# Kernel tuning notes

Hardware: AMD Instinct MI355X
Metric: run time of the kernel (lower is better)

Reference implementation:

```python
import jax, jax.numpy as jnp
import numpy as np

B, S, D, H = 8, 1024, 1024, 16
DH = D // H  # 64
SCALE = (DH // H) ** (-0.5)  # faithful to torch: (key.size(-1) // num_heads) ** -0.5 = 4**-0.5 = 0.5
LN_EPS = 1e-5


def setup_inputs() -> dict:
    key = jax.random.key(0)
    ks = jax.random.split(key, 12)
    f = jnp.float32
    return {
        "key":   jax.random.normal(ks[0], (B, S, D), f),
        "value": jax.random.normal(ks[1], (B, S, D), f),
        "query": jax.random.normal(ks[2], (B, S, D), f),
        "Wq": jax.random.normal(ks[3], (D, D), f) * 0.02,
        "bq": jnp.zeros((D,), f),
        "Wk": jax.random.normal(ks[4], (D, D), f) * 0.02,
        "bk": jnp.zeros((D,), f),
        "Wv": jax.random.normal(ks[5], (D, D), f) * 0.02,
        "bv": jnp.zeros((D,), f),
        "Wo": jax.random.normal(ks[6], (D, D), f) * 0.02,
        "bo": jnp.zeros((D,), f),
        "ln_gamma": jnp.ones((D,), f),
        "ln_beta": jnp.zeros((D,), f),
    }


def _layer_norm(x, gamma, beta):
    mu = jnp.mean(x, axis=-1, keepdims=True)
    var = jnp.mean(jnp.square(x - mu), axis=-1, keepdims=True)
    return (x - mu) * jax.lax.rsqrt(var + LN_EPS) * gamma + beta


def reference(key, value, query, Wq, bq, Wk, bk, Wv, bv, Wo, bo, ln_gamma, ln_beta):
    residual = query
    # QKV projections (torch Linear: x @ W.T + b)
    k = key @ Wk.T + bk
    v = value @ Wv.T + bv
    q = query @ Wq.T + bq
    # Faithful raw view [B,S,H*dh] -> [B*H, S, dh] (row-major reshape, as in torch .view)
    k = k.reshape(B * H, S, DH)
    v = v.reshape(B * H, S, DH)
    q = q.reshape(B * H, S, DH)
    # scores: [B*H, S, S], softmax over last axis (dim=2)
    attn = jnp.einsum("bid,bjd->bij", q, k) * SCALE
    attn = jax.nn.softmax(attn, axis=2)
    context = jnp.einsum("bij,bjd->bid", attn, v)
    context = context.reshape(B, S, D)  # faithful raw view back
    out = context @ Wo.T + bo
    out = _layer_norm(residual + out, ln_gamma, ln_beta)
    return out, attn
```

## Files before the change

kernel.cpp:

```cpp
#include <hip/hip_runtime.h>
#include <stdint.h>

typedef unsigned short ushort_t;
typedef __attribute__((ext_vector_type(8))) short s16x8;
typedef __attribute__((ext_vector_type(8))) unsigned short u16x8;
typedef __attribute__((ext_vector_type(4))) unsigned short u16x4;
typedef __attribute__((ext_vector_type(4))) float f32x4;

#define AS1C(p) ((const __attribute__((address_space(1))) void*)(p))
#define AS3(p)  ((__attribute__((address_space(3))) void*)(p))

#define QSCALE 0.7213475204444817f

#define EXP2F(x) __builtin_amdgcn_exp2f(x)
#define LOG2F(x) __builtin_amdgcn_logf(x)

#define WAVE_LDS_FENCE()                                    \
  do {                                                      \
    asm volatile("s_waitcnt lgkmcnt(0)" ::: "memory");      \
    __builtin_amdgcn_sched_barrier(0);                      \
  } while (0)

#define SBAR()                                              \
  do {                                                      \
    __builtin_amdgcn_sched_barrier(0);                      \
    __builtin_amdgcn_s_barrier();                           \
    __builtin_amdgcn_sched_barrier(0);                      \
  } while (0)

__device__ __forceinline__ ushort_t f2bf(float f) {
  uint32_t u = __float_as_uint(f);
  u += 0x7fffu + ((u >> 16) & 1u);
  return (ushort_t)(u >> 16);
}
__device__ __forceinline__ float bf2f(ushort_t h) {
  return __uint_as_float(((uint32_t)h) << 16);
}

__global__ __launch_bounds__(256) void cvt3_kernel(const float* __restrict__ s0,
                                                   const float* __restrict__ s1,
                                                   const float* __restrict__ s2,
                                                   ushort_t* __restrict__ dst) {
  const int y = blockIdx.y;
  const float* src = y == 0 ? s0 : (y == 1 ? s1 : s2);
  const int i = blockIdx.x * 256 + threadIdx.x;
  const float4 v = ((const float4*)src)[i];
  ushort4 o;
  o.x = f2bf(v.x); o.y = f2bf(v.y); o.z = f2bf(v.z); o.w = f2bf(v.w);
  ((ushort4*)(dst + (size_t)y * 8388608))[i] = o;
}

__global__ __launch_bounds__(256) void cvtw_kernel(const float* __restrict__ w0,
                                                   const float* __restrict__ w1,
                                                   const float* __restrict__ w2,
                                                   const float* __restrict__ w3,
                                                   ushort_t* __restrict__ dqkv,
                                                   ushort_t* __restrict__ dwo) {
  const int y = blockIdx.y;
  const float* src = y == 0 ? w0 : (y == 1 ? w1 : (y == 2 ? w2 : w3));
  ushort_t* dst = y < 3 ? dqkv + (size_t)y * 1048576 : dwo;
  const float sc = y == 0 ? QSCALE : 1.0f;
  const int i = blockIdx.x * 256 + threadIdx.x;
  const float4 v = ((const float4*)src)[i];
  ushort4 o;
  o.x = f2bf(v.x * sc); o.y = f2bf(v.y * sc); o.z = f2bf(v.z * sc); o.w = f2bf(v.w * sc);
  ((ushort4*)dst)[i] = o;
}

__global__ __launch_bounds__(256) void biascat_kernel(const float* __restrict__ bq,
                                                      const float* __restrict__ bk,
                                                      const float* __restrict__ bv,
                                                      float* __restrict__ dst) {
  const int i = blockIdx.x * 256 + threadIdx.x;
  dst[i] = i < 1024 ? bq[i] * QSCALE : (i < 2048 ? bk[i - 1024] : bv[i - 2048]);
}

template <int OUT_BF16>
__global__ __launch_bounds__(512) void gemm_nt(const ushort_t* __restrict__ A0,
                                               const ushort_t* __restrict__ A1,
                                               const ushort_t* __restrict__ A2,
                                               const ushort_t* __restrict__ B,
                                               const float* __restrict__ bias,
                                               void* __restrict__ C0,
                                               void* __restrict__ C1,
                                               void* __restrict__ C2) {
  __shared__ ushort_t As[3][128 * 32];
  __shared__ ushort_t Bs[3][128 * 32];
  const int tid = threadIdx.x;
  const int w = tid >> 6, lane = tid & 63, g = lane >> 4, c = lane & 15;
  const int wm = w >> 1, wn = w & 1;
  const int m0 = blockIdx.y * 128, n0 = blockIdx.x * 128;
  const int sel = n0 >> 10, nloc0 = n0 & 1023;
  const ushort_t* A = sel == 0 ? A0 : (sel == 1 ? A1 : A2);
  char* C = (char*)(sel == 0 ? C0 : (sel == 1 ? C1 : C2));
  f32x4 acc[2][4] = {};

  const int srow = tid >> 2, scol = (tid & 3) << 3;
  const int sdst = (w * 64) * 8;

#define G_STAGE(buf, k0_)                                                                  \
  do {                                                                                     \
    __builtin_amdgcn_global_load_lds(AS1C(&A[(size_t)(m0 + srow) * 1024 + (k0_) + scol]),  \
                                     AS3(&As[buf][sdst]), 16, 0, 0);                       \
    __builtin_amdgcn_global_load_lds(AS1C(&B[(size_t)(n0 + srow) * 1024 + (k0_) + scol]),  \
                                     AS3(&Bs[buf][sdst]), 16, 0, 0);                       \
  } while (0)

  G_STAGE(0, 0);
  G_STAGE(1, 32);
  asm volatile("s_waitcnt vmcnt(2)" ::: "memory");
  SBAR();
  int cur = 0;
  for (int it = 0; it < 32; ++it) {
    if (it < 30) {
      const int sb = cur >= 1 ? cur - 1 : 2;
      G_STAGE(sb, 32 * (it + 2));
    }
    s16x8 af[2], bfr[4];
#pragma unroll
    for (int mi = 0; mi < 2; ++mi)
      af[mi] = *(const s16x8*)&As[cur][(wm * 32 + mi * 16 + c) * 32 + g * 8];
#pragma unroll
    for (int ni = 0; ni < 4; ++ni)
      bfr[ni] = *(const s16x8*)&Bs[cur][(wn * 64 + ni * 16 + c) * 32 + g * 8];
    __builtin_amdgcn_s_setprio(1);
#pragma unroll
    for (int mi = 0; mi < 2; ++mi)
#pragma unroll
      for (int ni = 0; ni < 4; ++ni)
        acc[mi][ni] = __builtin_amdgcn_mfma_f32_16x16x32_bf16(af[mi], bfr[ni], acc[mi][ni], 0, 0, 0);
    __builtin_amdgcn_s_setprio(0);
    if (it < 31) {
      if (it < 30)
        asm volatile("s_waitcnt vmcnt(2) lgkmcnt(0)" ::: "memory");
      else
        asm volatile("s_waitcnt vmcnt(0) lgkmcnt(0)" ::: "memory");
      SBAR();
    }
    cur = cur < 2 ? cur + 1 : 0;
  }
#undef G_STAGE

#pragma unroll
  for (int ni = 0; ni < 4; ++ni) {
    const int nn = wn * 64 + ni * 16 + c;
    const float bv = bias[n0 + nn];
#pragma unroll
    for (int mi = 0; mi < 2; ++mi) {
#pragma unroll
      for (int rr = 0; rr < 4; ++rr) {
        const int m = m0 + wm * 32 + mi * 16 + g * 4 + rr;
        const float val = acc[mi][ni][rr] + bv;
        if (OUT_BF16)
          ((ushort_t*)C)[(size_t)m * 1024 + nloc0 + nn] = f2bf(val);
        else
          ((float*)C)[(size_t)m * 1024 + nloc0 + nn] = val;
      }
    }
  }
}

__global__ __launch_bounds__(256) void transpose_v(const ushort_t* __restrict__ v,
                                                   ushort_t* __restrict__ vt) {
  __shared__ ushort_t T[64][72];
  const int n = blockIdx.y, ib = blockIdx.x;
  const int t = threadIdx.x;
  {
    const int row = t >> 2, cb = (t & 3) << 4;
    const ushort_t* src = v + (size_t)n * 65536 + (size_t)(ib * 64 + row) * 64 + cb;
    *(u16x8*)&T[row][cb] = *(const u16x8*)src;
    *(u16x8*)&T[row][cb + 8] = *(const u16x8*)(src + 8);
  }
  __syncthreads();
  {
    const int dh = t >> 2, ibs = (t & 3) << 4;
    u16x8 a, b;
#pragma unroll
    for (int e = 0; e < 8; ++e) { a[e] = T[ibs + e][dh]; b[e] = T[ibs + 8 + e][dh]; }
    ushort_t* dst = vt + (size_t)n * 65536 + (size_t)dh * 1024 + ib * 64 + ibs;
    *(u16x8*)dst = a;
    *(u16x8*)(dst + 8) = b;
  }
}

__global__ __launch_bounds__(256) void stats_kernel(const ushort_t* __restrict__ q,
                                                    const ushort_t* __restrict__ k,
                                                    float* __restrict__ bias_out) {
  __shared__ ushort_t Kb[3][64 * 64];
  const int wg = blockIdx.x;
  const int idx = ((wg & 7) << 7) | (wg >> 3);
  const int n = idx >> 3, qb = idx & 7;
  const int tid = threadIdx.x, w = tid >> 6, lane = tid & 63, g = lane >> 4, c = lane & 15;
  const int q0 = qb * 128 + w * 32;
  const ushort_t* qh = q + (size_t)n * 65536;
  const char* khb = (const char*)(k + (size_t)n * 65536);

  const int r0 = w * 16 + (lane >> 3);
  const int csw = (((lane & 7) ^ (lane >> 3)) << 4);

#define STAGE_KS(buf, jt_)                                                                  \
  do {                                                                                      \
    __builtin_amdgcn_global_load_lds(AS1C(khb + ((size_t)(jt_)*64 + r0) * 128 + csw),       \
                                     AS3(&Kb[buf][(w * 2 + 0) * 512]), 16, 0, 0);           \
    __builtin_amdgcn_global_load_lds(AS1C(khb + ((size_t)(jt_)*64 + r0 + 8) * 128 + csw),   \
                                     AS3(&Kb[buf][(w * 2 + 1) * 512]), 16, 0, 0);           \
  } while (0)
#define KFRAGS(buf, jn, h)                                                    \
  (*(const s16x8*)((const char*)&Kb[buf][0] +                                 \
                   (((((jn)*16 + c) * 128 + (h)*64 + g * 16)) ^ ((c & 7) << 4))))

  s16x8 aq[2][2];
#pragma unroll
  for (int fr = 0; fr < 2; ++fr) {
    aq[fr][0] = *(const s16x8*)&qh[(q0 + fr * 16 + c) * 64 + g * 8];
    aq[fr][1] = *(const s16x8*)&qh[(q0 + fr * 16 + c) * 64 + 32 + g * 8];
  }

  float l_acc[2][4] = {};

  STAGE_KS(0, 0);
  STAGE_KS(1, 1);
  asm volatile("s_waitcnt vmcnt(2)" ::: "memory");
  SBAR();
  int cur = 0;
  for (int jt = 0; jt < 16; ++jt) {
    if (jt < 14) {
      const int sb = cur >= 1 ? cur - 1 : 2;
      STAGE_KS(sb, jt + 2);
    }
    f32x4 sfr[2][4];
    __builtin_amdgcn_s_setprio(1);
#pragma unroll
    for (int fr = 0; fr < 2; ++fr)
#pragma unroll
      for (int jn = 0; jn < 4; ++jn) {
        f32x4 z = {0.f, 0.f, 0.f, 0.f};
        z = __builtin_amdgcn_mfma_f32_16x16x32_bf16(aq[fr][0], KFRAGS(cur, jn, 0), z, 0, 0, 0);
        z = __builtin_amdgcn_mfma_f32_16x16x32_bf16(aq[fr][1], KFRAGS(cur, jn, 1), z, 0, 0, 0);
        sfr[fr][jn] = z;
      }
    __builtin_amdgcn_s_setprio(0);
#pragma unroll
    for (int fr = 0; fr < 2; ++fr)
#pragma unroll
      for (int rr = 0; rr < 4; ++rr)
        l_acc[fr][rr] += EXP2F(sfr[fr][0][rr]) + EXP2F(sfr[fr][1][rr]) +
                         EXP2F(sfr[fr][2][rr]) + EXP2F(sfr[fr][3][rr]);
    if (jt < 15) {
      if (jt < 14)
        asm volatile("s_waitcnt vmcnt(2) lgkmcnt(0)" ::: "memory");
      else
        asm volatile("s_waitcnt vmcnt(0) lgkmcnt(0)" ::: "memory");
      SBAR();
    }
    cur = cur < 2 ? cur + 1 : 0;
  }

#pragma unroll
  for (int fr = 0; fr < 2; ++fr)
#pragma unroll
    for (int rr = 0; rr < 4; ++rr) {
      float l = l_acc[fr][rr];
      l += __shfl_xor(l, 1);
      l += __shfl_xor(l, 2);
      l += __shfl_xor(l, 4);
      l += __shfl_xor(l, 8);
      if (c == 0)
        bias_out[(size_t)n * 1024 + q0 + fr * 16 + g * 4 + rr] = LOG2F(l);
    }
#undef STAGE_KS
#undef KFRAGS
}

__global__ __launch_bounds__(256) void attn_kernel(const ushort_t* __restrict__ q,
                                                   const ushort_t* __restrict__ k,
                                                   const ushort_t* __restrict__ vt,
                                                   const float* __restrict__ stats,
                                                   float* __restrict__ attn,
                                                   ushort_t* __restrict__ ctx) {
  __shared__ ushort_t Kb[2][64 * 64];
  __shared__ ushort_t Vb[2][64 * 64];
  __shared__ ushort_t Pb[4][32 * 64];
  const int wg = blockIdx.x;
  const int idx = ((wg & 7) << 7) | (wg >> 3);
  const int n = idx >> 3, qb = idx & 7;
  const int tid = threadIdx.x, w = tid >> 6, lane = tid & 63, g = lane >> 4, c = lane & 15;
  const int i0 = qb * 128 + w * 32;
  const ushort_t* qh = q + (size_t)n * 65536;
  const char* khb = (const char*)(k + (size_t)n * 65536);
  const char* vhb = (const char*)(vt + (size_t)n * 65536);
  char* pwb = (char*)&Pb[w][0];

  const int r0 = w * 16 + (lane >> 3);
  const int csw = (((lane & 7) ^ (lane >> 3)) << 4);

#define STAGE_K(buf, jt_)                                                                   \
  do {                                                                                      \
    __builtin_amdgcn_global_load_lds(AS1C(khb + ((size_t)(jt_)*64 + r0) * 128 + csw),       \
                                     AS3(&Kb[buf][(w * 2 + 0) * 512]), 16, 0, 0);           \
    __builtin_amdgcn_global_load_lds(AS1C(khb + ((size_t)(jt_)*64 + r0 + 8) * 128 + csw),   \
                                     AS3(&Kb[buf][(w * 2 + 1) * 512]), 16, 0, 0);           \
  } while (0)
#define STAGE_V(buf, jt_)                                                                   \
  do {                                                                                      \
    __builtin_amdgcn_global_load_lds(AS1C(vhb + (size_t)r0 * 2048 + (jt_)*128 + csw),       \
                                     AS3(&Vb[buf][(w * 2 + 0) * 512]), 16, 0, 0);           \
    __builtin_amdgcn_global_load_lds(AS1C(vhb + (size_t)(r0 + 8) * 2048 + (jt_)*128 + csw), \
                                     AS3(&Vb[buf][(w * 2 + 1) * 512]), 16, 0, 0);           \
  } while (0)
#define KFRAG(buf, jn, h)                                                     \
  (*(const s16x8*)((const char*)&Kb[buf][0] +                                 \
                   (((((jn)*16 + c) * 128 + (h)*64 + g * 16)) ^ ((c & 7) << 4))))
#define VFRAG(buf, dn, ks_)                                                   \
  (*(const s16x8*)((const char*)&Vb[buf][0] +                                 \
                   (((((dn)*16 + c) * 128 + (ks_)*64 + g * 16)) ^ ((c & 7) << 4))))

  s16x8 aq[2][2];
  float bias_r[2][4];
#pragma unroll
  for (int fr = 0; fr < 2; ++fr) {
    aq[fr][0] = *(const s16x8*)&qh[(i0 + fr * 16 + c) * 64 + g * 8];
    aq[fr][1] = *(const s16x8*)&qh[(i0 + fr * 16 + c) * 64 + 32 + g * 8];
    const float* sb = stats + (size_t)n * 1024 + i0 + fr * 16;
#pragma unroll
    for (int r = 0; r < 4; ++r) bias_r[fr][r] = sb[4 * g + r];
  }

  f32x4 cacc[2][4] = {};
  float* arow = attn + (size_t)n * 1048576;

  STAGE_K(0, 0);
  STAGE_V(0, 0);
  asm volatile("s_waitcnt vmcnt(0) lgkmcnt(0)" ::: "memory");
  SBAR();
  for (int jt = 0; jt < 16; ++jt) {
    const int cur = jt & 1;
    if (jt < 15) { STAGE_K(cur ^ 1, jt + 1); STAGE_V(cur ^ 1, jt + 1); }
    f32x4 s[2][4];
    __builtin_amdgcn_s_setprio(1);
#pragma unroll
    for (int fr = 0; fr < 2; ++fr)
#pragma unroll
      for (int jn = 0; jn < 4; ++jn) {
        f32x4 z = {0.f, 0.f, 0.f, 0.f};
        z = __builtin_amdgcn_mfma_f32_16x16x32_bf16(aq[fr][0], KFRAG(cur, jn, 0), z, 0, 0, 0);
        z = __builtin_amdgcn_mfma_f32_16x16x32_bf16(aq[fr][1], KFRAG(cur, jn, 1), z, 0, 0, 0);
        s[fr][jn] = z;
      }
    __builtin_amdgcn_s_setprio(0);
#pragma unroll
    for (int fr = 0; fr < 2; ++fr)
#pragma unroll
      for (int jn = 0; jn < 4; ++jn)
#pragma unroll
        for (int r = 0; r < 4; ++r) {
          const float p = EXP2F(s[fr][jn][r] - bias_r[fr][r]);
          const int row = fr * 16 + 4 * g + r;
          const int A = (row << 7) + ((jn * 16 + c) << 1);
          *(ushort_t*)(pwb + (A ^ ((row & 7) << 4))) = f2bf(p);
        }
    WAVE_LDS_FENCE();
    __builtin_amdgcn_s_setprio(1);
#pragma unroll
    for (int ks = 0; ks < 2; ++ks) {
      s16x8 pa[2];
#pragma unroll
      for (int fr = 0; fr < 2; ++fr) {
        const int A = ((fr * 16 + c) << 7) + (ks << 6) + (g << 4);
        pa[fr] = *(const s16x8*)(pwb + (A ^ ((c & 7) << 4)));
      }
#pragma unroll
      for (int dn = 0; dn < 4; ++dn) {
        const s16x8 bv = VFRAG(cur, dn, ks);
        cacc[0][dn] = __builtin_amdgcn_mfma_f32_16x16x32_bf16(pa[0], bv, cacc[0][dn], 0, 0, 0);
        cacc[1][dn] = __builtin_amdgcn_mfma_f32_16x16x32_bf16(pa[1], bv, cacc[1][dn], 0, 0, 0);
      }
    }
    __builtin_amdgcn_s_setprio(0);
#pragma unroll
    for (int fr = 0; fr < 2; ++fr)
#pragma unroll
      for (int e = 0; e < 4; ++e) {
        const int row = fr * 16 + g + 4 * e;
        const int A = (row << 7) + (c << 3);
        const u16x4 hv = *(const u16x4*)(pwb + (A ^ ((row & 7) << 4)));
        f32x4 fv;
#pragma unroll
        for (int t2 = 0; t2 < 4; ++t2) fv[t2] = bf2f(hv[t2]);
        __builtin_nontemporal_store(
            fv, (f32x4*)&arow[(size_t)(i0 + row) * 1024 + jt * 64 + c * 4]);
      }
    if (jt < 15) {
      asm volatile("s_waitcnt vmcnt(8) lgkmcnt(0)" ::: "memory");
      SBAR();
    }
  }

  ushort_t* ch = ctx + (size_t)n * 65536;
#pragma unroll
  for (int fr = 0; fr < 2; ++fr)
#pragma unroll
    for (int dn = 0; dn < 4; ++dn)
#pragma unroll
      for (int r = 0; r < 4; ++r)
        ch[(size_t)(i0 + fr * 16 + 4 * g + r) * 64 + dn * 16 + c] = f2bf(cacc[fr][dn][r]);
#undef STAGE_K
#undef STAGE_V
#undef KFRAG
#undef VFRAG
}

__global__ __launch_bounds__(256) void ln_kernel(const float* __restrict__ proj,
                                                 const float* __restrict__ resid,
                                                 const float* __restrict__ gamma,
                                                 const float* __restrict__ beta,
                                                 float* __restrict__ out) {
  __shared__ float sred[4], ssred[4];
  const int row = blockIdx.x, t = threadIdx.x;
  const float4 pv = ((const float4*)(proj + (size_t)row * 1024))[t];
  const float4 rv = ((const float4*)(resid + (size_t)row * 1024))[t];
  float4 x;
  x.x = pv.x + rv.x; x.y = pv.y + rv.y; x.z = pv.z + rv.z; x.w = pv.w + rv.w;
  float s = x.x + x.y + x.z + x.w;
  float ss = x.x * x.x + x.y * x.y + x.z * x.z + x.w * x.w;
#pragma unroll
  for (int msk = 1; msk < 64; msk <<= 1) {
    s += __shfl_xor(s, msk);
    ss += __shfl_xor(ss, msk);
  }
  const int w = t >> 6, lane = t & 63;
  if (lane == 0) { sred[w] = s; ssred[w] = ss; }
  __syncthreads();
  s = sred[0] + sred[1] + sred[2] + sred[3];
  ss = ssred[0] + ssred[1] + ssred[2] + ssred[3];
  const float mu = s * (1.f / 1024.f);
  const float var = ss * (1.f / 1024.f) - mu * mu;
  const float rs = rsqrtf(var + 1e-5f);
  const float4 gm = ((const float4*)gamma)[t];
  const float4 bt = ((const float4*)beta)[t];
  float4 o;
  o.x = (x.x - mu) * rs * gm.x + bt.x;
  o.y = (x.y - mu) * rs * gm.y + bt.y;
  o.z = (x.z - mu) * rs * gm.z + bt.z;
  o.w = (x.w - mu) * rs * gm.w + bt.w;
  ((float4*)(out + (size_t)row * 1024))[t] = o;
}

extern "C" void kernel_launch(void* const* d_in, const int* in_sizes, int n_in,
                              void* d_out, int out_size, void* d_ws, size_t ws_size,
                              hipStream_t stream) {
  const float* key   = (const float*)d_in[0];
  const float* value = (const float*)d_in[1];
  const float* query = (const float*)d_in[2];
  const float* Wq = (const float*)d_in[3];  const float* bq = (const float*)d_in[4];
  const float* Wk = (const float*)d_in[5];  const float* bk = (const float*)d_in[6];
  const float* Wv = (const float*)d_in[7];  const float* bv = (const float*)d_in[8];
  const float* Wo = (const float*)d_in[9];  const float* bo = (const float*)d_in[10];
  const float* gamma = (const float*)d_in[11];
  const float* beta  = (const float*)d_in[12];

  char* ws = (char*)d_ws;
  ushort_t* q_   = (ushort_t*)(ws + 0);
  ushort_t* k_   = (ushort_t*)(ws + 16777216);
  ushort_t* vt_  = (ushort_t*)(ws + 33554432);
  ushort_t* ctx_ = (ushort_t*)(ws + 50331648);
  ushort_t* wo_  = (ushort_t*)(ws + 67108864);
  float*    proj_ = (float*)(ws + 0);

  char* o8 = (char*)d_out;
  float*    outp  = (float*)o8;
  float*    attnp = (float*)(o8 + 33554432);
  float*    stats = (float*)o8;
  ushort_t* xq   = (ushort_t*)(o8 + 33554432);
  ushort_t* xk   = (ushort_t*)(o8 + 50331648);
  ushort_t* xv   = (ushort_t*)(o8 + 67108864);
  ushort_t* wqkv = (ushort_t*)(o8 + 83886080);
  ushort_t* v_   = (ushort_t*)(o8 + 90177536);
  float*    bqkv = (float*)(o8 + 106954752);

  cvt3_kernel<<<dim3(8192, 3), 256, 0, stream>>>(query, key, value, xq);
  cvtw_kernel<<<dim3(1024, 4), 256, 0, stream>>>(Wq, Wk, Wv, Wo, wqkv, wo_);
  biascat_kernel<<<12, 256, 0, stream>>>(bq, bk, bv, bqkv);

  gemm_nt<1><<<dim3(24, 64), 512, 0, stream>>>(xq, xk, xv, wqkv, bqkv, q_, k_, v_);

  transpose_v<<<dim3(16, 128), 256, 0, stream>>>(v_, vt_);

  stats_kernel<<<1024, 256, 0, stream>>>(q_, k_, stats);

  attn_kernel<<<1024, 256, 0, stream>>>(q_, k_, vt_, stats, attnp, ctx_);

  gemm_nt<0><<<dim3(8, 64), 512, 0, stream>>>(ctx_, ctx_, ctx_, wo_, bo, proj_, proj_, proj_);

  ln_kernel<<<8192, 256, 0, stream>>>(proj_, query, gamma, beta, outp);
}
```

Baseline: 314.0 us.

## Swap MFMA operands so P stays in registers, double stats tile

In the attention kernel the QK^T MFMA operands are swapped, so each lane holds a row's scores along the key dimension. The probabilities are written straight to the attn output as fp32 vectors and packed to bf16, then rearranged with cross-lane shuffles into the B operand of the PV MFMA (also with swapped operands). This removes the per-wave LDS P buffer, the LDS round-trip and the bf16 readback for the attn store, and the attn output now keeps full fp32 precision instead of bf16-rounded values. Separately, the stats kernel handles 64 query rows per wave with half as many blocks, reusing each staged K tile across more rows.

Measured after the change: 392.3 us. 1.25x slower.

```diff
diff --git a/kernel.cpp b/kernel.cpp
--- a/kernel.cpp
+++ b/kernel.cpp
@@ -6,6 +6,7 @@
 typedef __attribute__((ext_vector_type(8))) unsigned short u16x8;
 typedef __attribute__((ext_vector_type(4))) unsigned short u16x4;
 typedef __attribute__((ext_vector_type(4))) float f32x4;
+typedef __attribute__((ext_vector_type(4))) unsigned int u32x4;
 
 #define AS1C(p) ((const __attribute__((address_space(1))) void*)(p))
 #define AS3(p)  ((__attribute__((address_space(3))) void*)(p))
@@ -14,12 +15,6 @@
 
 #define EXP2F(x) __builtin_amdgcn_exp2f(x)
 #define LOG2F(x) __builtin_amdgcn_logf(x)
-
-#define WAVE_LDS_FENCE()                                    \
-  do {                                                      \
-    asm volatile("s_waitcnt lgkmcnt(0)" ::: "memory");      \
-    __builtin_amdgcn_sched_barrier(0);                      \
-  } while (0)
 
 #define SBAR()                                              \
   do {                                                      \
@@ -33,8 +28,8 @@
   u += 0x7fffu + ((u >> 16) & 1u);
   return (ushort_t)(u >> 16);
 }
-__device__ __forceinline__ float bf2f(ushort_t h) {
-  return __uint_as_float(((uint32_t)h) << 16);
+__device__ __forceinline__ uint32_t packbf(float lo, float hi) {
+  return (uint32_t)f2bf(lo) | ((uint32_t)f2bf(hi) << 16);
 }
 
 __global__ __launch_bounds__(256) void cvt3_kernel(const float* __restrict__ s0,
@@ -188,10 +183,10 @@
                                                     float* __restrict__ bias_out) {
   __shared__ ushort_t Kb[3][64 * 64];
   const int wg = blockIdx.x;
-  const int idx = ((wg & 7) << 7) | (wg >> 3);
-  const int n = idx >> 3, qb = idx & 7;
+  const int idx = ((wg & 7) << 6) | (wg >> 3);
+  const int n = idx >> 2, qb = idx & 3;
   const int tid = threadIdx.x, w = tid >> 6, lane = tid & 63, g = lane >> 4, c = lane & 15;
-  const int q0 = qb * 128 + w * 32;
+  const int q0 = qb * 256 + w * 64;
   const ushort_t* qh = q + (size_t)n * 65536;
   const char* khb = (const char*)(k + (size_t)n * 65536);
 
@@ -209,14 +204,14 @@
   (*(const s16x8*)((const char*)&Kb[buf][0] +                                 \
                    (((((jn)*16 + c) * 128 + (h)*64 + g * 16)) ^ ((c & 7) << 4))))
 
-  s16x8 aq[2][2];
-#pragma unroll
-  for (int fr = 0; fr < 2; ++fr) {
+  s16x8 aq[4][2];
+#pragma unroll
+  for (int fr = 0; fr < 4; ++fr) {
     aq[fr][0] = *(const s16x8*)&qh[(q0 + fr * 16 + c) * 64 + g * 8];
     aq[fr][1] = *(const s16x8*)&qh[(q0 + fr * 16 + c) * 64 + 32 + g * 8];
   }
 
-  float l_acc[2][4] = {};
+  float l_acc[4][4] = {};
 
   STAGE_KS(0, 0);
   STAGE_KS(1, 1);
@@ -228,24 +223,23 @@
       const int sb = cur >= 1 ? cur - 1 : 2;
       STAGE_KS(sb, jt + 2);
     }
-    f32x4 sfr[2][4];
-    __builtin_amdgcn_s_setprio(1);
-#pragma unroll
-    for (int fr = 0; fr < 2; ++fr)
+#pragma unroll
+    for (int fr = 0; fr < 4; ++fr) {
+      f32x4 sfr[4];
+      __builtin_amdgcn_s_setprio(1);
 #pragma unroll
       for (int jn = 0; jn < 4; ++jn) {
         f32x4 z = {0.f, 0.f, 0.f, 0.f};
         z = __builtin_amdgcn_mfma_f32_16x16x32_bf16(aq[fr][0], KFRAGS(cur, jn, 0), z, 0, 0, 0);
         z = __builtin_amdgcn_mfma_f32_16x16x32_bf16(aq[fr][1], KFRAGS(cur, jn, 1), z, 0, 0, 0);
-        sfr[fr][jn] = z;
+        sfr[jn] = z;
       }
-    __builtin_amdgcn_s_setprio(0);
-#pragma unroll
-    for (int fr = 0; fr < 2; ++fr)
+      __builtin_amdgcn_s_setprio(0);
 #pragma unroll
       for (int rr = 0; rr < 4; ++rr)
-        l_acc[fr][rr] += EXP2F(sfr[fr][0][rr]) + EXP2F(sfr[fr][1][rr]) +
-                         EXP2F(sfr[fr][2][rr]) + EXP2F(sfr[fr][3][rr]);
+        l_acc[fr][rr] += EXP2F(sfr[0][rr]) + EXP2F(sfr[1][rr]) +
+                         EXP2F(sfr[2][rr]) + EXP2F(sfr[3][rr]);
+    }
     if (jt < 15) {
       if (jt < 14)
         asm volatile("s_waitcnt vmcnt(2) lgkmcnt(0)" ::: "memory");
@@ -257,7 +251,7 @@
   }
 
 #pragma unroll
-  for (int fr = 0; fr < 2; ++fr)
+  for (int fr = 0; fr < 4; ++fr)
 #pragma unroll
     for (int rr = 0; rr < 4; ++rr) {
       float l = l_acc[fr][rr];
@@ -280,7 +274,6 @@
                                                    ushort_t* __restrict__ ctx) {
   __shared__ ushort_t Kb[2][64 * 64];
   __shared__ ushort_t Vb[2][64 * 64];
-  __shared__ ushort_t Pb[4][32 * 64];
   const int wg = blockIdx.x;
   const int idx = ((wg & 7) << 7) | (wg >> 3);
   const int n = idx >> 3, qb = idx & 7;
@@ -289,7 +282,6 @@
   const ushort_t* qh = q + (size_t)n * 65536;
   const char* khb = (const char*)(k + (size_t)n * 65536);
   const char* vhb = (const char*)(vt + (size_t)n * 65536);
-  char* pwb = (char*)&Pb[w][0];
 
   const int r0 = w * 16 + (lane >> 3);
   const int csw = (((lane & 7) ^ (lane >> 3)) << 4);
@@ -316,15 +308,17 @@
                    (((((dn)*16 + c) * 128 + (ks_)*64 + g * 16)) ^ ((c & 7) << 4))))
 
   s16x8 aq[2][2];
-  float bias_r[2][4];
+  float bias_f[2];
 #pragma unroll
   for (int fr = 0; fr < 2; ++fr) {
     aq[fr][0] = *(const s16x8*)&qh[(i0 + fr * 16 + c) * 64 + g * 8];
     aq[fr][1] = *(const s16x8*)&qh[(i0 + fr * 16 + c) * 64 + 32 + g * 8];
-    const float* sb = stats + (size_t)n * 1024 + i0 + fr * 16;
-#pragma unroll
-    for (int r = 0; r < 4; ++r) bias_r[fr][r] = sb[4 * g + r];
-  }
+    bias_f[fr] = stats[(size_t)n * 1024 + i0 + fr * 16 + c];
+  }
+
+  const int srcA = (lane & 15) + ((lane >> 4) & 1) * 32;
+  const int srcB = srcA + 16;
+  const bool hi = lane >= 32;
 
   f32x4 cacc[2][4] = {};
   float* arow = attn + (size_t)n * 1048576;
@@ -343,53 +337,49 @@
 #pragma unroll
       for (int jn = 0; jn < 4; ++jn) {
         f32x4 z = {0.f, 0.f, 0.f, 0.f};
-        z = __builtin_amdgcn_mfma_f32_16x16x32_bf16(aq[fr][0], KFRAG(cur, jn, 0), z, 0, 0, 0);
-        z = __builtin_amdgcn_mfma_f32_16x16x32_bf16(aq[fr][1], KFRAG(cur, jn, 1), z, 0, 0, 0);
+        z = __builtin_amdgcn_mfma_f32_16x16x32_bf16(KFRAG(cur, jn, 0), aq[fr][0], z, 0, 0, 0);
+        z = __builtin_amdgcn_mfma_f32_16x16x32_bf16(KFRAG(cur, jn, 1), aq[fr][1], z, 0, 0, 0);
         s[fr][jn] = z;
       }
     __builtin_amdgcn_s_setprio(0);
+    uint32_t pk[2][4][2];
 #pragma unroll
     for (int fr = 0; fr < 2; ++fr)
 #pragma unroll
-      for (int jn = 0; jn < 4; ++jn)
-#pragma unroll
-        for (int r = 0; r < 4; ++r) {
-          const float p = EXP2F(s[fr][jn][r] - bias_r[fr][r]);
-          const int row = fr * 16 + 4 * g + r;
-          const int A = (row << 7) + ((jn * 16 + c) << 1);
-          *(ushort_t*)(pwb + (A ^ ((row & 7) << 4))) = f2bf(p);
-        }
-    WAVE_LDS_FENCE();
+      for (int jn = 0; jn < 4; ++jn) {
+        f32x4 pv;
+#pragma unroll
+        for (int r = 0; r < 4; ++r) pv[r] = EXP2F(s[fr][jn][r] - bias_f[fr]);
+        __builtin_nontemporal_store(
+            pv, (f32x4*)&arow[(size_t)(i0 + fr * 16 + c) * 1024 + jt * 64 + jn * 16 + g * 4]);
+        pk[fr][jn][0] = packbf(pv[0], pv[1]);
+        pk[fr][jn][1] = packbf(pv[2], pv[3]);
+      }
     __builtin_amdgcn_s_setprio(1);
 #pragma unroll
-    for (int ks = 0; ks < 2; ++ks) {
-      s16x8 pa[2];
-#pragma unroll
-      for (int fr = 0; fr < 2; ++fr) {
-        const int A = ((fr * 16 + c) << 7) + (ks << 6) + (g << 4);
-        pa[fr] = *(const s16x8*)(pwb + (A ^ ((c & 7) << 4)));
+    for (int fr = 0; fr < 2; ++fr)
+#pragma unroll
+      for (int ks = 0; ks < 2; ++ks) {
+        const uint32_t a0 = __shfl(pk[fr][2 * ks][0], srcA);
+        const uint32_t a1 = __shfl(pk[fr][2 * ks + 1][0], srcA);
+        const uint32_t b0 = __shfl(pk[fr][2 * ks][1], srcA);
+        const uint32_t b1 = __shfl(pk[fr][2 * ks + 1][1], srcA);
+        const uint32_t c0 = __shfl(pk[fr][2 * ks][0], srcB);
+        const uint32_t c1 = __shfl(pk[fr][2 * ks + 1][0], srcB);
+        const uint32_t d0 = __shfl(pk[fr][2 * ks][1], srcB);
+        const uint32_t d1 = __shfl(pk[fr][2 * ks + 1][1], srcB);
+        u32x4 wv;
+        wv[0] = hi ? a1 : a0;
+        wv[1] = hi ? b1 : b0;
+        wv[2] = hi ? c1 : c0;
+        wv[3] = hi ? d1 : d0;
+        const s16x8 pb = __builtin_bit_cast(s16x8, wv);
+#pragma unroll
+        for (int dn = 0; dn < 4; ++dn)
+          cacc[fr][dn] =
+              __builtin_amdgcn_mfma_f32_16x16x32_bf16(VFRAG(cur, dn, ks), pb, cacc[fr][dn], 0, 0, 0);
       }
-#pragma unroll
-      for (int dn = 0; dn < 4; ++dn) {
-        const s16x8 bv = VFRAG(cur, dn, ks);
-        cacc[0][dn] = __builtin_amdgcn_mfma_f32_16x16x32_bf16(pa[0], bv, cacc[0][dn], 0, 0, 0);
-        cacc[1][dn] = __builtin_amdgcn_mfma_f32_16x16x32_bf16(pa[1], bv, cacc[1][dn], 0, 0, 0);
-      }
-    }
     __builtin_amdgcn_s_setprio(0);
-#pragma unroll
-    for (int fr = 0; fr < 2; ++fr)
-#pragma unroll
-      for (int e = 0; e < 4; ++e) {
-        const int row = fr * 16 + g + 4 * e;
-        const int A = (row << 7) + (c << 3);
-        const u16x4 hv = *(const u16x4*)(pwb + (A ^ ((row & 7) << 4)));
-        f32x4 fv;
-#pragma unroll
-        for (int t2 = 0; t2 < 4; ++t2) fv[t2] = bf2f(hv[t2]);
-        __builtin_nontemporal_store(
-            fv, (f32x4*)&arow[(size_t)(i0 + row) * 1024 + jt * 64 + c * 4]);
-      }
     if (jt < 15) {
       asm volatile("s_waitcnt vmcnt(8) lgkmcnt(0)" ::: "memory");
       SBAR();
@@ -400,10 +390,14 @@
 #pragma unroll
   for (int fr = 0; fr < 2; ++fr)
 #pragma unroll
-    for (int dn = 0; dn < 4; ++dn)
-#pragma unroll
-      for (int r = 0; r < 4; ++r)
-        ch[(size_t)(i0 + fr * 16 + 4 * g + r) * 64 + dn * 16 + c] = f2bf(cacc[fr][dn][r]);
+    for (int dn = 0; dn < 4; ++dn) {
+      ushort4 o;
+      o.x = f2bf(cacc[fr][dn][0]);
+      o.y = f2bf(cacc[fr][dn][1]);
+      o.z = f2bf(cacc[fr][dn][2]);
+      o.w = f2bf(cacc[fr][dn][3]);
+      *(ushort4*)&ch[(size_t)(i0 + fr * 16 + c) * 64 + dn * 16 + g * 4] = o;
+    }
 #undef STAGE_K
 #undef STAGE_V
 #undef KFRAG
@@ -486,7 +480,7 @@
 
   transpose_v<<<dim3(16, 128), 256, 0, stream>>>(v_, vt_);
 
-  stats_kernel<<<1024, 256, 0, stream>>>(q_, k_, stats);
+  stats_kernel<<<512, 256, 0, stream>>>(q_, k_, stats);
 
   attn_kernel<<<1024, 256, 0, stream>>>(q_, k_, vt_, stats, attnp, ctx_);
 
```

## Double stats rows per block and halve attention P staging buffer

Applied to the files above, without the earlier changes.

The stats kernel now gives each wave 64 query rows instead of 32 and launches 512 blocks instead of 1024, so every staged K tile is reused across twice as many rows and the total K traffic for the row sums is halved. The attention kernel now handles its two 16-row fragments one after another through a half-size per-wave P buffer in LDS, with an extra wave-level fence between them, which cuts its LDS footprint. The trade-offs are more registers and fewer blocks in the stats kernel, and extra serialization between the two fragments in the attention kernel.

New measurement: 319.3 us. Within noise of the previous version (+1.7%).

```diff
diff --git a/kernel.cpp b/kernel.cpp
--- a/kernel.cpp
+++ b/kernel.cpp
@@ -188,10 +188,10 @@
                                                     float* __restrict__ bias_out) {
   __shared__ ushort_t Kb[3][64 * 64];
   const int wg = blockIdx.x;
-  const int idx = ((wg & 7) << 7) | (wg >> 3);
-  const int n = idx >> 3, qb = idx & 7;
+  const int idx = ((wg & 7) << 6) | (wg >> 3);
+  const int n = idx >> 2, qb = idx & 3;
   const int tid = threadIdx.x, w = tid >> 6, lane = tid & 63, g = lane >> 4, c = lane & 15;
-  const int q0 = qb * 128 + w * 32;
+  const int q0 = qb * 256 + w * 64;
   const ushort_t* qh = q + (size_t)n * 65536;
   const char* khb = (const char*)(k + (size_t)n * 65536);
 
@@ -209,14 +209,14 @@
   (*(const s16x8*)((const char*)&Kb[buf][0] +                                 \
                    (((((jn)*16 + c) * 128 + (h)*64 + g * 16)) ^ ((c & 7) << 4))))
 
-  s16x8 aq[2][2];
-#pragma unroll
-  for (int fr = 0; fr < 2; ++fr) {
+  s16x8 aq[4][2];
+#pragma unroll
+  for (int fr = 0; fr < 4; ++fr) {
     aq[fr][0] = *(const s16x8*)&qh[(q0 + fr * 16 + c) * 64 + g * 8];
     aq[fr][1] = *(const s16x8*)&qh[(q0 + fr * 16 + c) * 64 + 32 + g * 8];
   }
 
-  float l_acc[2][4] = {};
+  float l_acc[4][4] = {};
 
   STAGE_KS(0, 0);
   STAGE_KS(1, 1);
@@ -228,24 +228,23 @@
       const int sb = cur >= 1 ? cur - 1 : 2;
       STAGE_KS(sb, jt + 2);
     }
-    f32x4 sfr[2][4];
-    __builtin_amdgcn_s_setprio(1);
-#pragma unroll
-    for (int fr = 0; fr < 2; ++fr)
+#pragma unroll
+    for (int fr = 0; fr < 4; ++fr) {
+      f32x4 sfr[4];
+      __builtin_amdgcn_s_setprio(1);
 #pragma unroll
       for (int jn = 0; jn < 4; ++jn) {
         f32x4 z = {0.f, 0.f, 0.f, 0.f};
         z = __builtin_amdgcn_mfma_f32_16x16x32_bf16(aq[fr][0], KFRAGS(cur, jn, 0), z, 0, 0, 0);
         z = __builtin_amdgcn_mfma_f32_16x16x32_bf16(aq[fr][1], KFRAGS(cur, jn, 1), z, 0, 0, 0);
-        sfr[fr][jn] = z;
+        sfr[jn] = z;
       }
-    __builtin_amdgcn_s_setprio(0);
-#pragma unroll
-    for (int fr = 0; fr < 2; ++fr)
+      __builtin_amdgcn_s_setprio(0);
 #pragma unroll
       for (int rr = 0; rr < 4; ++rr)
-        l_acc[fr][rr] += EXP2F(sfr[fr][0][rr]) + EXP2F(sfr[fr][1][rr]) +
-                         EXP2F(sfr[fr][2][rr]) + EXP2F(sfr[fr][3][rr]);
+        l_acc[fr][rr] += EXP2F(sfr[0][rr]) + EXP2F(sfr[1][rr]) +
+                         EXP2F(sfr[2][rr]) + EXP2F(sfr[3][rr]);
+    }
     if (jt < 15) {
       if (jt < 14)
         asm volatile("s_waitcnt vmcnt(2) lgkmcnt(0)" ::: "memory");
@@ -257,7 +256,7 @@
   }
 
 #pragma unroll
-  for (int fr = 0; fr < 2; ++fr)
+  for (int fr = 0; fr < 4; ++fr)
 #pragma unroll
     for (int rr = 0; rr < 4; ++rr) {
       float l = l_acc[fr][rr];
@@ -280,7 +279,7 @@
                                                    ushort_t* __restrict__ ctx) {
   __shared__ ushort_t Kb[2][64 * 64];
   __shared__ ushort_t Vb[2][64 * 64];
-  __shared__ ushort_t Pb[4][32 * 64];
+  __shared__ ushort_t Pb[4][16 * 64];
   const int wg = blockIdx.x;
   const int idx = ((wg & 7) << 7) | (wg >> 3);
   const int n = idx >> 3, qb = idx & 7;
@@ -349,47 +348,41 @@
       }
     __builtin_amdgcn_s_setprio(0);
 #pragma unroll
-    for (int fr = 0; fr < 2; ++fr)
+    for (int fr = 0; fr < 2; ++fr) {
 #pragma unroll
       for (int jn = 0; jn < 4; ++jn)
 #pragma unroll
         for (int r = 0; r < 4; ++r) {
           const float p = EXP2F(s[fr][jn][r] - bias_r[fr][r]);
-          const int row = fr * 16 + 4 * g + r;
+          const int row = 4 * g + r;
           const int A = (row << 7) + ((jn * 16 + c) << 1);
           *(ushort_t*)(pwb + (A ^ ((row & 7) << 4))) = f2bf(p);
         }
-    WAVE_LDS_FENCE();
-    __builtin_amdgcn_s_setprio(1);
-#pragma unroll
-    for (int ks = 0; ks < 2; ++ks) {
-      s16x8 pa[2];
-#pragma unroll
-      for (int fr = 0; fr < 2; ++fr) {
-        const int A = ((fr * 16 + c) << 7) + (ks << 6) + (g << 4);
-        pa[fr] = *(const s16x8*)(pwb + (A ^ ((c & 7) << 4)));
+      WAVE_LDS_FENCE();
+      __builtin_amdgcn_s_setprio(1);
+#pragma unroll
+      for (int ks = 0; ks < 2; ++ks) {
+        const int A = (c << 7) + (ks << 6) + (g << 4);
+        const s16x8 pa = *(const s16x8*)(pwb + (A ^ ((c & 7) << 4)));
+#pragma unroll
+        for (int dn = 0; dn < 4; ++dn)
+          cacc[fr][dn] =
+              __builtin_amdgcn_mfma_f32_16x16x32_bf16(pa, VFRAG(cur, dn, ks), cacc[fr][dn], 0, 0, 0);
       }
-#pragma unroll
-      for (int dn = 0; dn < 4; ++dn) {
-        const s16x8 bv = VFRAG(cur, dn, ks);
-        cacc[0][dn] = __builtin_amdgcn_mfma_f32_16x16x32_bf16(pa[0], bv, cacc[0][dn], 0, 0, 0);
-        cacc[1][dn] = __builtin_amdgcn_mfma_f32_16x16x32_bf16(pa[1], bv, cacc[1][dn], 0, 0, 0);
-      }
-    }
-    __builtin_amdgcn_s_setprio(0);
-#pragma unroll
-    for (int fr = 0; fr < 2; ++fr)
+      __builtin_amdgcn_s_setprio(0);
 #pragma unroll
       for (int e = 0; e < 4; ++e) {
-        const int row = fr * 16 + g + 4 * e;
+        const int row = g + 4 * e;
         const int A = (row << 7) + (c << 3);
         const u16x4 hv = *(const u16x4*)(pwb + (A ^ ((row & 7) << 4)));
         f32x4 fv;
 #pragma unroll
         for (int t2 = 0; t2 < 4; ++t2) fv[t2] = bf2f(hv[t2]);
         __builtin_nontemporal_store(
-            fv, (f32x4*)&arow[(size_t)(i0 + row) * 1024 + jt * 64 + c * 4]);
+            fv, (f32x4*)&arow[(size_t)(i0 + fr * 16 + row) * 1024 + jt * 64 + c * 4]);
       }
+      WAVE_LDS_FENCE();
+    }
     if (jt < 15) {
       asm volatile("s_waitcnt vmcnt(8) lgkmcnt(0)" ::: "memory");
       SBAR();
@@ -486,7 +479,7 @@
 
   transpose_v<<<dim3(16, 128), 256, 0, stream>>>(v_, vt_);
 
-  stats_kernel<<<1024, 256, 0, stream>>>(q_, k_, stats);
+  stats_kernel<<<512, 256, 0, stream>>>(q_, k_, stats);
 
   attn_kernel<<<1024, 256, 0, stream>>>(q_, k_, vt_, stats, attnp, ctx_);
 
```
